# Performance work log

Hardware: AMD Instinct MI355X
Metric: run time of the kernel (lower is better)

Reference implementation:

```python
import jax, jax.numpy as jnp
import numpy as np

LN_EPS = 1e-5

def _layernorm(x, g, b):
    mu = jnp.mean(x, axis=-1, keepdims=True)
    var = jnp.var(x, axis=-1, keepdims=True)
    return (x - mu) * jax.lax.rsqrt(var + LN_EPS) * g + b

def setup_inputs() -> dict:
    key = jax.random.key(0)
    ks = jax.random.split(key, 12)
    B, E, R = 32, 64, 36
    Dt, Di, D = 768, 2048, 512
    s = 0.02
    return {
        "text_feats": jax.random.normal(ks[0], (B, E, Dt), jnp.float32),
        "image_feats": jax.random.normal(ks[1], (B, R, Di), jnp.float32),
        "W_text": jax.random.normal(ks[2], (Dt, D), jnp.float32) * s,
        "b_text": jnp.zeros((D,), jnp.float32),
        "g_text": jnp.ones((D,), jnp.float32),
        "beta_text": jnp.zeros((D,), jnp.float32),
        "W_img": jax.random.normal(ks[3], (Di, D), jnp.float32) * s,
        "b_img": jnp.zeros((D,), jnp.float32),
        "g_img": jnp.ones((D,), jnp.float32),
        "beta_img": jnp.zeros((D,), jnp.float32),
        "W1": jax.random.normal(ks[4], (2 * D, D), jnp.float32) * s,
        "b1": jnp.zeros((D,), jnp.float32),
        "W2": jax.random.normal(ks[5], (D, 1), jnp.float32) * s,
        "b2": jnp.zeros((1,), jnp.float32),
    }

def reference(text_feats, image_feats, W_text, b_text, g_text, beta_text,
              W_img, b_img, g_img, beta_img, W1, b1, W2, b2):
    B, E, _ = text_feats.shape
    R = image_feats.shape[1]
    D = W_text.shape[1]
    # projections: Linear -> ReLU -> LayerNorm
    text_aligned = _layernorm(jax.nn.relu(text_feats @ W_text + b_text), g_text, beta_text)   # [B,E,D]
    image_aligned = _layernorm(jax.nn.relu(image_feats @ W_img + b_img), g_img, beta_img)     # [B,R,D]
    # pairwise scorer: split W1 to avoid materializing the [B,E,R,2D] concat
    W1_t, W1_i = W1[:D], W1[D:]
    h_t = text_aligned @ W1_t                 # [B,E,D]
    h_i = image_aligned @ W1_i + b1           # [B,R,D]
    h = jax.nn.relu(h_t[:, :, None, :] + h_i[:, None, :, :])  # [B,E,R,D]
    scores_raw = jnp.squeeze(h @ W2, -1) + b2[0]               # [B,E,R]
    alignment_scores = jax.nn.sigmoid(scores_raw)
    # softmax over flattened (E*R) per batch
    w = jax.nn.softmax(alignment_scores.reshape(B, E * R), axis=1).reshape(B, E, R)
    # weighted sum over regions, mean over entities
    aggregated = jnp.einsum('ber,brd->bd', w, image_aligned) / E   # [B,D]
    return alignment_scores, aggregated
```

## Files before the change

### kernel.cpp

```cpp
#include <hip/hip_runtime.h>
#include <math.h>

#define LN_EPS 1e-5f

typedef __attribute__((ext_vector_type(8))) short bf16x8;
typedef __attribute__((ext_vector_type(4))) float f32x4;
typedef unsigned short ushort_t;
typedef unsigned int uint_t;

__device__ __forceinline__ ushort_t f2bf(float f) {
    uint_t u = __float_as_uint(f);
    u += 0x7FFF + ((u >> 16) & 1);
    return (ushort_t)(u >> 16);
}

__global__ __launch_bounds__(256) void prep_kernel(
    const float* __restrict__ text, const float* __restrict__ image,
    ushort_t* __restrict__ text_bf, ushort_t* __restrict__ image_bf,
    const float* __restrict__ W_text, const float* __restrict__ W_img,
    const float* __restrict__ W1,
    ushort_t* __restrict__ Wt_t, ushort_t* __restrict__ Wi_t,
    ushort_t* __restrict__ W1t_t, ushort_t* __restrict__ W1i_t)
{
    __shared__ float t[32][33];
    const int bid = blockIdx.x;
    if (bid < 3840) {
        const int i4 = (bid * 256 + threadIdx.x) * 4;
        const float* src; ushort_t* dst; int off;
        if (i4 < 1572864) { src = text;  dst = text_bf;  off = i4; }
        else              { src = image; dst = image_bf; off = i4 - 1572864; }
        float4 v = *(const float4*)(src + off);
        ushort4 o;
        o.x = f2bf(v.x); o.y = f2bf(v.y); o.z = f2bf(v.z); o.w = f2bf(v.w);
        *(ushort4*)(dst + off) = o;
        return;
    }
    int local = bid - 3840;
    const float* src; ushort_t* dst; int K;
    if      (local < 384)  { src = W_text;         dst = Wt_t;  K = 768;  }
    else if (local < 1408) { src = W_img;          dst = Wi_t;  K = 2048; local -= 384; }
    else if (local < 1664) { src = W1;             dst = W1t_t; K = 512;  local -= 1408; }
    else                   { src = W1 + 512 * 512; dst = W1i_t; K = 512;  local -= 1664; }
    const int ntk = K / 32;
    const int k0 = (local % ntk) * 32;
    const int n0 = (local / ntk) * 32;
    const int x = threadIdx.x % 32, y = threadIdx.x / 32;
    #pragma unroll
    for (int j = 0; j < 4; ++j)
        t[y + 8 * j][x] = src[(size_t)(k0 + y + 8 * j) * 512 + n0 + x];
    __syncthreads();
    #pragma unroll
    for (int j = 0; j < 4; ++j)
        dst[(size_t)(n0 + y + 8 * j) * K + k0 + x] = f2bf(t[x][y + 8 * j]);
}

__global__ __launch_bounds__(256) void gemm_splitk_kernel(
    const ushort_t* __restrict__ A0, const ushort_t* __restrict__ B0,
    const float* __restrict__ bias0, float* __restrict__ C0, int K0,
    const ushort_t* __restrict__ A1, const ushort_t* __restrict__ B1,
    const float* __restrict__ bias1, float* __restrict__ C1, int K1,
    int ysplit, int relu)
{
    __shared__ float red[4][64][64];

    const ushort_t* A; const ushort_t* Bt; const float* bias; float* C; int K;
    int yy = blockIdx.y;
    if (yy < ysplit) { A = A0; Bt = B0; bias = bias0; C = C0; K = K0; }
    else { A = A1; Bt = B1; bias = bias1; C = C1; K = K1; yy -= ysplit; }

    const int tid  = threadIdx.x;
    const int wave = tid >> 6;
    const int lane = tid & 63;
    const int q    = lane >> 4;
    const int mj   = lane & 15;
    const int brow = yy * 64;
    const int bcol = blockIdx.x * 64;

    const ushort_t* Ab = A  + (size_t)(brow + mj) * K + q * 8;
    const ushort_t* Bb = Bt + (size_t)(bcol + mj) * K + q * 8;
    const int kw0    = wave * (K >> 2);
    const int ksteps = K >> 7;

    f32x4 acc[4][4] = {};

    #pragma unroll 2
    for (int s = 0; s < ksteps; ++s) {
        const int k = kw0 + s * 32;
        bf16x8 af[4], bf[4];
        #pragma unroll
        for (int i = 0; i < 4; ++i) {
            af[i] = *(const bf16x8*)(Ab + (size_t)i * 16 * K + k);
            bf[i] = *(const bf16x8*)(Bb + (size_t)i * 16 * K + k);
        }
        #pragma unroll
        for (int mi = 0; mi < 4; ++mi)
            #pragma unroll
            for (int ni = 0; ni < 4; ++ni)
                acc[mi][ni] = __builtin_amdgcn_mfma_f32_16x16x32_bf16(
                    af[mi], bf[ni], acc[mi][ni], 0, 0, 0);
    }

    #pragma unroll
    for (int mi = 0; mi < 4; ++mi)
        #pragma unroll
        for (int ni = 0; ni < 4; ++ni)
            #pragma unroll
            for (int r = 0; r < 4; ++r)
                red[wave][mi * 16 + q * 4 + r][ni * 16 + mj] = acc[mi][ni][r];
    __syncthreads();

    #pragma unroll
    for (int g = 0; g < 4; ++g) {
        const int idx = g * 1024 + tid * 4;
        const int row = idx >> 6, col = idx & 63;
        float4 v0 = *(float4*)&red[0][row][col];
        float4 v1 = *(float4*)&red[1][row][col];
        float4 v2 = *(float4*)&red[2][row][col];
        float4 v3 = *(float4*)&red[3][row][col];
        float4 o;
        o.x = (v0.x + v1.x) + (v2.x + v3.x);
        o.y = (v0.y + v1.y) + (v2.y + v3.y);
        o.z = (v0.z + v1.z) + (v2.z + v3.z);
        o.w = (v0.w + v1.w) + (v2.w + v3.w);
        if (bias) {
            float4 bv = *(const float4*)&bias[bcol + col];
            o.x += bv.x; o.y += bv.y; o.z += bv.z; o.w += bv.w;
        }
        if (relu) {
            o.x = fmaxf(o.x, 0.f); o.y = fmaxf(o.y, 0.f);
            o.z = fmaxf(o.z, 0.f); o.w = fmaxf(o.w, 0.f);
        }
        *(float4*)&C[(size_t)(brow + row) * 512 + bcol + col] = o;
    }
}

__global__ __launch_bounds__(256) void ln_fused_kernel(
    float* __restrict__ ta, const float* __restrict__ g_t,
    const float* __restrict__ be_t, ushort_t* __restrict__ ta_bf,
    float* __restrict__ ia, const float* __restrict__ g_i,
    const float* __restrict__ be_i, ushort_t* __restrict__ ia_bf)
{
    const int tid = threadIdx.x;
    int row = blockIdx.x;
    float* p; const float* g; const float* beta; ushort_t* obf; float* ofp;
    if (row < 2048) {
        p = ta + (size_t)row * 512; g = g_t; beta = be_t;
        obf = ta_bf + (size_t)row * 512; ofp = nullptr;
    } else {
        row -= 2048;
        p = ia + (size_t)row * 512; g = g_i; beta = be_i;
        obf = ia_bf + (size_t)row * 512; ofp = p;
    }

    float2 v = *(const float2*)&p[tid * 2];
    float s  = v.x + v.y;
    float ss = v.x * v.x + v.y * v.y;
    #pragma unroll
    for (int off = 32; off; off >>= 1) {
        s  += __shfl_down(s, off);
        ss += __shfl_down(ss, off);
    }
    __shared__ float red[8];
    if ((tid & 63) == 0) { red[(tid >> 6) * 2] = s; red[(tid >> 6) * 2 + 1] = ss; }
    __syncthreads();
    __shared__ float stats[2];
    if (tid == 0) {
        float S  = red[0] + red[2] + red[4] + red[6];
        float SS = red[1] + red[3] + red[5] + red[7];
        float mu  = S * (1.f / 512.f);
        float var = SS * (1.f / 512.f) - mu * mu;
        stats[0] = mu;
        stats[1] = rsqrtf(var + LN_EPS);
    }
    __syncthreads();
    const float mu = stats[0], rstd = stats[1];
    float2 gv = *(const float2*)&g[tid * 2];
    float2 bv = *(const float2*)&beta[tid * 2];
    float o0 = (v.x - mu) * rstd * gv.x + bv.x;
    float o1 = (v.y - mu) * rstd * gv.y + bv.y;
    ushort2 ob; ob.x = f2bf(o0); ob.y = f2bf(o1);
    *(ushort2*)&obf[tid * 2] = ob;
    if (ofp) {
        float2 of; of.x = o0; of.y = o1;
        *(float2*)&ofp[tid * 2] = of;
    }
}

__global__ __launch_bounds__(256) void scores_kernel(
    const float* __restrict__ ht, const float* __restrict__ hi,
    const float* __restrict__ W2, const float* __restrict__ b2,
    float* __restrict__ scores)
{
    const int be   = blockIdx.x;
    const int b    = be >> 6;
    const int tid  = threadIdx.x;
    const int lane = tid & 63;
    const int wave = tid >> 6;

    float htv[8], w2v[8];
    const float* htp = ht + (size_t)be * 512;
    #pragma unroll
    for (int j = 0; j < 8; ++j) {
        htv[j] = htp[lane + 64 * j];
        w2v[j] = W2[lane + 64 * j];
    }
    const float bb = b2[0];
    const float* hib = hi + (size_t)b * 36 * 512;

    for (int r = wave; r < 36; r += 4) {
        const float* hir = hib + (size_t)r * 512;
        float acc = 0.f;
        #pragma unroll
        for (int j = 0; j < 8; ++j) {
            float h = fmaxf(htv[j] + hir[lane + 64 * j], 0.f);
            acc = fmaf(h, w2v[j], acc);
        }
        #pragma unroll
        for (int off = 32; off; off >>= 1) acc += __shfl_down(acc, off);
        if (lane == 0) {
            float sr = acc + bb;
            scores[(size_t)be * 36 + r] = 1.f / (1.f + expf(-sr));
        }
    }
}

__global__ __launch_bounds__(256) void agg_kernel(
    const float* __restrict__ scores, const float* __restrict__ img,
    float* __restrict__ outAgg)
{
    const int b   = blockIdx.x;
    const int tid = threadIdx.x;
    const float* sc = scores + (size_t)b * 2304;

    __shared__ float part[4][36];
    __shared__ float sexp[36];
    __shared__ float inv_s;

    const int e4 = tid >> 6;
    const int r  = tid & 63;
    if (r < 36) {
        float p = 0.f;
        #pragma unroll
        for (int e = 0; e < 16; ++e) p += expf(sc[(e * 4 + e4) * 36 + r]);
        part[e4][r] = p;
    }
    __syncthreads();
    if (tid < 36) sexp[tid] = part[0][tid] + part[1][tid] + part[2][tid] + part[3][tid];
    __syncthreads();
    if (tid < 64) {
        float v = (tid < 36) ? sexp[tid] : 0.f;
        #pragma unroll
        for (int off = 32; off; off >>= 1) v += __shfl_down(v, off);
        if (tid == 0) inv_s = 1.f / (v * 64.f);
    }
    __syncthreads();
    const float inv = inv_s;

    const float* ib = img + (size_t)b * 36 * 512;
    for (int d = tid; d < 512; d += 256) {
        float acc = 0.f;
        #pragma unroll
        for (int rr = 0; rr < 36; ++rr)
            acc = fmaf(sexp[rr] * inv, ib[rr * 512 + d], acc);
        outAgg[(size_t)b * 512 + d] = acc;
    }
}

extern "C" void kernel_launch(void* const* d_in, const int* in_sizes, int n_in,
                              void* d_out, int out_size, void* d_ws, size_t ws_size,
                              hipStream_t stream)
{
    const float* text      = (const float*)d_in[0];
    const float* image     = (const float*)d_in[1];
    const float* W_text    = (const float*)d_in[2];
    const float* b_text    = (const float*)d_in[3];
    const float* g_text    = (const float*)d_in[4];
    const float* beta_text = (const float*)d_in[5];
    const float* W_img     = (const float*)d_in[6];
    const float* b_img     = (const float*)d_in[7];
    const float* g_img     = (const float*)d_in[8];
    const float* beta_img  = (const float*)d_in[9];
    const float* W1        = (const float*)d_in[10];
    const float* b1        = (const float*)d_in[11];
    const float* W2        = (const float*)d_in[12];
    const float* b2        = (const float*)d_in[13];

    float* out_scores = (float*)d_out;
    float* out_agg    = (float*)d_out + 73728;

    char* ws = (char*)d_ws;
    float*    ta       = (float*)(ws);
    float*    ia       = (float*)(ws + (4u << 20));
    ushort_t* text_bf  = (ushort_t*)(ws + 6402048);
    ushort_t* image_bf = (ushort_t*)(ws + 6402048 + 3145728);
    float*    ht       = (float*)(ws + 6402048);
    float*    hi       = (float*)(ws + 6402048 + 4194304);
    char*     wbase    = ws + 6402048 + 7864320;
    ushort_t* Wt_t     = (ushort_t*)(wbase);
    ushort_t* Wi_t     = (ushort_t*)(wbase + 786432);
    ushort_t* W1t_t    = (ushort_t*)(wbase + 786432 + 2097152);
    ushort_t* W1i_t    = (ushort_t*)(wbase + 786432 + 2097152 + 524288);
    char*     bfbase   = wbase + 786432 + 2097152 + 2 * 524288;
    ushort_t* ta_bf    = (ushort_t*)(bfbase);
    ushort_t* ia_bf    = (ushort_t*)(bfbase + 2097152);

    prep_kernel<<<5760, 256, 0, stream>>>(text, image, text_bf, image_bf,
                                          W_text, W_img, W1,
                                          Wt_t, Wi_t, W1t_t, W1i_t);
    gemm_splitk_kernel<<<dim3(8, 50), 256, 0, stream>>>(
        text_bf, Wt_t, b_text, ta, 768,
        image_bf, Wi_t, b_img, ia, 2048,
        32, 1);
    ln_fused_kernel<<<3200, 256, 0, stream>>>(ta, g_text, beta_text, ta_bf,
                                              ia, g_img, beta_img, ia_bf);
    gemm_splitk_kernel<<<dim3(8, 50), 256, 0, stream>>>(
        ta_bf, W1t_t, nullptr, ht, 512,
        ia_bf, W1i_t, b1, hi, 512,
        32, 0);
    scores_kernel<<<2048, 256, 0, stream>>>(ht, hi, W2, b2, out_scores);
    agg_kernel<<<32, 256, 0, stream>>>(out_scores, ia, out_agg);
}
```

Before: 148.0 us.

## Fuse bf16 casts, LayerNorm stats and normalization into GEMM prologues/epilogues

```diff
diff --git a/kernel.cpp b/kernel.cpp
--- a/kernel.cpp
+++ b/kernel.cpp
@@ -14,28 +14,28 @@
     return (ushort_t)(u >> 16);
 }
 
+__device__ __forceinline__ bf16x8 cvt8(float4 a, float4 b) {
+    bf16x8 r;
+    r[0] = (short)f2bf(a.x); r[1] = (short)f2bf(a.y);
+    r[2] = (short)f2bf(a.z); r[3] = (short)f2bf(a.w);
+    r[4] = (short)f2bf(b.x); r[5] = (short)f2bf(b.y);
+    r[6] = (short)f2bf(b.z); r[7] = (short)f2bf(b.w);
+    return r;
+}
+
 __global__ __launch_bounds__(256) void prep_kernel(
-    const float* __restrict__ text, const float* __restrict__ image,
-    ushort_t* __restrict__ text_bf, ushort_t* __restrict__ image_bf,
     const float* __restrict__ W_text, const float* __restrict__ W_img,
     const float* __restrict__ W1,
     ushort_t* __restrict__ Wt_t, ushort_t* __restrict__ Wi_t,
-    ushort_t* __restrict__ W1t_t, ushort_t* __restrict__ W1i_t)
+    ushort_t* __restrict__ W1t_t, ushort_t* __restrict__ W1i_t,
+    float* __restrict__ stats)
 {
     __shared__ float t[32][33];
-    const int bid = blockIdx.x;
-    if (bid < 3840) {
-        const int i4 = (bid * 256 + threadIdx.x) * 4;
-        const float* src; ushort_t* dst; int off;
-        if (i4 < 1572864) { src = text;  dst = text_bf;  off = i4; }
-        else              { src = image; dst = image_bf; off = i4 - 1572864; }
-        float4 v = *(const float4*)(src + off);
-        ushort4 o;
-        o.x = f2bf(v.x); o.y = f2bf(v.y); o.z = f2bf(v.z); o.w = f2bf(v.w);
-        *(ushort4*)(dst + off) = o;
+    int local = blockIdx.x;
+    if (local >= 1920) {
+        for (int i = threadIdx.x; i < 6400; i += 256) stats[i] = 0.f;
         return;
     }
-    int local = bid - 3840;
     const float* src; ushort_t* dst; int K;
     if      (local < 384)  { src = W_text;         dst = Wt_t;  K = 768;  }
     else if (local < 1408) { src = W_img;          dst = Wi_t;  K = 2048; local -= 384; }
@@ -54,19 +54,19 @@
         dst[(size_t)(n0 + y + 8 * j) * K + k0 + x] = f2bf(t[x][y + 8 * j]);
 }
 
-__global__ __launch_bounds__(256) void gemm_splitk_kernel(
-    const ushort_t* __restrict__ A0, const ushort_t* __restrict__ B0,
+__global__ __launch_bounds__(256) void proj_kernel(
+    const float* __restrict__ A0, const ushort_t* __restrict__ B0,
     const float* __restrict__ bias0, float* __restrict__ C0, int K0,
-    const ushort_t* __restrict__ A1, const ushort_t* __restrict__ B1,
+    const float* __restrict__ A1, const ushort_t* __restrict__ B1,
     const float* __restrict__ bias1, float* __restrict__ C1, int K1,
-    int ysplit, int relu)
+    float* __restrict__ stats, int ysplit)
 {
     __shared__ float red[4][64][64];
 
-    const ushort_t* A; const ushort_t* Bt; const float* bias; float* C; int K;
+    const float* A; const ushort_t* Bt; const float* bias; float* C; int K, srow;
     int yy = blockIdx.y;
-    if (yy < ysplit) { A = A0; Bt = B0; bias = bias0; C = C0; K = K0; }
-    else { A = A1; Bt = B1; bias = bias1; C = C1; K = K1; yy -= ysplit; }
+    if (yy < ysplit) { A = A0; Bt = B0; bias = bias0; C = C0; K = K0; srow = yy * 64; }
+    else { A = A1; Bt = B1; bias = bias1; C = C1; K = K1; yy -= ysplit; srow = 2048 + yy * 64; }
 
     const int tid  = threadIdx.x;
     const int wave = tid >> 6;
@@ -76,7 +76,7 @@
     const int brow = yy * 64;
     const int bcol = blockIdx.x * 64;
 
-    const ushort_t* Ab = A  + (size_t)(brow + mj) * K + q * 8;
+    const float*    Ab = A  + (size_t)(brow + mj) * K + q * 8;
     const ushort_t* Bb = Bt + (size_t)(bcol + mj) * K + q * 8;
     const int kw0    = wave * (K >> 2);
     const int ksteps = K >> 7;
@@ -89,7 +89,10 @@
         bf16x8 af[4], bf[4];
         #pragma unroll
         for (int i = 0; i < 4; ++i) {
-            af[i] = *(const bf16x8*)(Ab + (size_t)i * 16 * K + k);
+            const float* pA = Ab + (size_t)i * 16 * K + k;
+            float4 x0 = *(const float4*)pA;
+            float4 x1 = *(const float4*)(pA + 4);
+            af[i] = cvt8(x0, x1);
             bf[i] = *(const bf16x8*)(Bb + (size_t)i * 16 * K + k);
         }
         #pragma unroll
@@ -112,6 +115,118 @@
     #pragma unroll
     for (int g = 0; g < 4; ++g) {
         const int idx = g * 1024 + tid * 4;
+        const int row = idx >> 6, col = idx & 63;
+        float4 v0 = *(float4*)&red[0][row][col];
+        float4 v1 = *(float4*)&red[1][row][col];
+        float4 v2 = *(float4*)&red[2][row][col];
+        float4 v3 = *(float4*)&red[3][row][col];
+        float4 bv = *(const float4*)&bias[bcol + col];
+        float4 o;
+        o.x = fmaxf((v0.x + v1.x) + (v2.x + v3.x) + bv.x, 0.f);
+        o.y = fmaxf((v0.y + v1.y) + (v2.y + v3.y) + bv.y, 0.f);
+        o.z = fmaxf((v0.z + v1.z) + (v2.z + v3.z) + bv.z, 0.f);
+        o.w = fmaxf((v0.w + v1.w) + (v2.w + v3.w) + bv.w, 0.f);
+        *(float4*)&C[(size_t)(brow + row) * 512 + bcol + col] = o;
+        float s  = (o.x + o.y) + (o.z + o.w);
+        float ss = (o.x * o.x + o.y * o.y) + (o.z * o.z + o.w * o.w);
+        #pragma unroll
+        for (int m = 1; m < 16; m <<= 1) {
+            s  += __shfl_xor(s, m);
+            ss += __shfl_xor(ss, m);
+        }
+        if ((tid & 15) == 0) {
+            atomicAdd(&stats[(size_t)(srow + row) * 2], s);
+            atomicAdd(&stats[(size_t)(srow + row) * 2 + 1], ss);
+        }
+    }
+}
+
+__global__ __launch_bounds__(256) void h_kernel(
+    const float* __restrict__ A0, const ushort_t* __restrict__ B0,
+    const float* __restrict__ bias0, float* __restrict__ C0,
+    const float* __restrict__ g0, const float* __restrict__ be0, int soff0,
+    const float* __restrict__ A1, const ushort_t* __restrict__ B1,
+    const float* __restrict__ bias1, float* __restrict__ C1,
+    const float* __restrict__ g1, const float* __restrict__ be1, int soff1,
+    const float* __restrict__ stats, int ysplit)
+{
+    __shared__ float red[4][64][64];
+
+    const float* A; const ushort_t* Bt; const float* bias; float* C;
+    const float* g; const float* be; int soff;
+    int yy = blockIdx.y;
+    if (yy < ysplit) { A = A0; Bt = B0; bias = bias0; C = C0; g = g0; be = be0; soff = soff0; }
+    else { A = A1; Bt = B1; bias = bias1; C = C1; g = g1; be = be1; soff = soff1; yy -= ysplit; }
+
+    const int tid  = threadIdx.x;
+    const int wave = tid >> 6;
+    const int lane = tid & 63;
+    const int q    = lane >> 4;
+    const int mj   = lane & 15;
+    const int brow = yy * 64;
+    const int bcol = blockIdx.x * 64;
+
+    float mu[4], rstd[4];
+    #pragma unroll
+    for (int i = 0; i < 4; ++i) {
+        const int row = soff + brow + i * 16 + mj;
+        float2 st = *(const float2*)&stats[(size_t)row * 2];
+        float m   = st.x * (1.f / 512.f);
+        float var = st.y * (1.f / 512.f) - m * m;
+        mu[i] = m; rstd[i] = rsqrtf(var + LN_EPS);
+    }
+
+    const float*    Ab = A  + (size_t)(brow + mj) * 512 + q * 8;
+    const ushort_t* Bb = Bt + (size_t)(bcol + mj) * 512 + q * 8;
+    const int kw0 = wave * 128;
+
+    f32x4 acc[4][4] = {};
+
+    #pragma unroll 2
+    for (int s = 0; s < 4; ++s) {
+        const int k = kw0 + s * 32;
+        float4 gv0 = *(const float4*)&g[k + q * 8];
+        float4 gv1 = *(const float4*)&g[k + q * 8 + 4];
+        float4 bv0 = *(const float4*)&be[k + q * 8];
+        float4 bv1 = *(const float4*)&be[k + q * 8 + 4];
+        bf16x8 af[4], bf[4];
+        #pragma unroll
+        for (int i = 0; i < 4; ++i) {
+            const float* pA = Ab + (size_t)i * 16 * 512 + k;
+            float4 x0 = *(const float4*)pA;
+            float4 x1 = *(const float4*)(pA + 4);
+            float4 t0, t1;
+            t0.x = fmaf((x0.x - mu[i]) * rstd[i], gv0.x, bv0.x);
+            t0.y = fmaf((x0.y - mu[i]) * rstd[i], gv0.y, bv0.y);
+            t0.z = fmaf((x0.z - mu[i]) * rstd[i], gv0.z, bv0.z);
+            t0.w = fmaf((x0.w - mu[i]) * rstd[i], gv0.w, bv0.w);
+            t1.x = fmaf((x1.x - mu[i]) * rstd[i], gv1.x, bv1.x);
+            t1.y = fmaf((x1.y - mu[i]) * rstd[i], gv1.y, bv1.y);
+            t1.z = fmaf((x1.z - mu[i]) * rstd[i], gv1.z, bv1.z);
+            t1.w = fmaf((x1.w - mu[i]) * rstd[i], gv1.w, bv1.w);
+            af[i] = cvt8(t0, t1);
+            bf[i] = *(const bf16x8*)(Bb + (size_t)i * 16 * 512 + k);
+        }
+        #pragma unroll
+        for (int mi = 0; mi < 4; ++mi)
+            #pragma unroll
+            for (int ni = 0; ni < 4; ++ni)
+                acc[mi][ni] = __builtin_amdgcn_mfma_f32_16x16x32_bf16(
+                    af[mi], bf[ni], acc[mi][ni], 0, 0, 0);
+    }
+
+    #pragma unroll
+    for (int mi = 0; mi < 4; ++mi)
+        #pragma unroll
+        for (int ni = 0; ni < 4; ++ni)
+            #pragma unroll
+            for (int r = 0; r < 4; ++r)
+                red[wave][mi * 16 + q * 4 + r][ni * 16 + mj] = acc[mi][ni][r];
+    __syncthreads();
+
+    #pragma unroll
+    for (int gq = 0; gq < 4; ++gq) {
+        const int idx = gq * 1024 + tid * 4;
         const int row = idx >> 6, col = idx & 63;
         float4 v0 = *(float4*)&red[0][row][col];
         float4 v1 = *(float4*)&red[1][row][col];
@@ -126,63 +241,7 @@
             float4 bv = *(const float4*)&bias[bcol + col];
             o.x += bv.x; o.y += bv.y; o.z += bv.z; o.w += bv.w;
         }
-        if (relu) {
-            o.x = fmaxf(o.x, 0.f); o.y = fmaxf(o.y, 0.f);
-            o.z = fmaxf(o.z, 0.f); o.w = fmaxf(o.w, 0.f);
-        }
         *(float4*)&C[(size_t)(brow + row) * 512 + bcol + col] = o;
-    }
-}
-
-__global__ __launch_bounds__(256) void ln_fused_kernel(
-    float* __restrict__ ta, const float* __restrict__ g_t,
-    const float* __restrict__ be_t, ushort_t* __restrict__ ta_bf,
-    float* __restrict__ ia, const float* __restrict__ g_i,
-    const float* __restrict__ be_i, ushort_t* __restrict__ ia_bf)
-{
-    const int tid = threadIdx.x;
-    int row = blockIdx.x;
-    float* p; const float* g; const float* beta; ushort_t* obf; float* ofp;
-    if (row < 2048) {
-        p = ta + (size_t)row * 512; g = g_t; beta = be_t;
-        obf = ta_bf + (size_t)row * 512; ofp = nullptr;
-    } else {
-        row -= 2048;
-        p = ia + (size_t)row * 512; g = g_i; beta = be_i;
-        obf = ia_bf + (size_t)row * 512; ofp = p;
-    }
-
-    float2 v = *(const float2*)&p[tid * 2];
-    float s  = v.x + v.y;
-    float ss = v.x * v.x + v.y * v.y;
-    #pragma unroll
-    for (int off = 32; off; off >>= 1) {
-        s  += __shfl_down(s, off);
-        ss += __shfl_down(ss, off);
-    }
-    __shared__ float red[8];
-    if ((tid & 63) == 0) { red[(tid >> 6) * 2] = s; red[(tid >> 6) * 2 + 1] = ss; }
-    __syncthreads();
-    __shared__ float stats[2];
-    if (tid == 0) {
-        float S  = red[0] + red[2] + red[4] + red[6];
-        float SS = red[1] + red[3] + red[5] + red[7];
-        float mu  = S * (1.f / 512.f);
-        float var = SS * (1.f / 512.f) - mu * mu;
-        stats[0] = mu;
-        stats[1] = rsqrtf(var + LN_EPS);
-    }
-    __syncthreads();
-    const float mu = stats[0], rstd = stats[1];
-    float2 gv = *(const float2*)&g[tid * 2];
-    float2 bv = *(const float2*)&beta[tid * 2];
-    float o0 = (v.x - mu) * rstd * gv.x + bv.x;
-    float o1 = (v.y - mu) * rstd * gv.y + bv.y;
-    ushort2 ob; ob.x = f2bf(o0); ob.y = f2bf(o1);
-    *(ushort2*)&obf[tid * 2] = ob;
-    if (ofp) {
-        float2 of; of.x = o0; of.y = o1;
-        *(float2*)&ofp[tid * 2] = of;
     }
 }
 
@@ -191,41 +250,59 @@
     const float* __restrict__ W2, const float* __restrict__ b2,
     float* __restrict__ scores)
 {
-    const int be   = blockIdx.x;
-    const int b    = be >> 6;
+    const int blk  = blockIdx.x;
+    const int b    = blk >> 4;
+    const int e0   = (blk & 15) * 4;
     const int tid  = threadIdx.x;
     const int lane = tid & 63;
     const int wave = tid >> 6;
 
-    float htv[8], w2v[8];
-    const float* htp = ht + (size_t)be * 512;
-    #pragma unroll
-    for (int j = 0; j < 8; ++j) {
-        htv[j] = htp[lane + 64 * j];
-        w2v[j] = W2[lane + 64 * j];
-    }
+    float htv[4][8], w2v[8];
+    #pragma unroll
+    for (int e = 0; e < 4; ++e) {
+        const float* htp = ht + (size_t)(b * 64 + e0 + e) * 512;
+        #pragma unroll
+        for (int j = 0; j < 8; ++j) htv[e][j] = htp[lane + 64 * j];
+    }
+    #pragma unroll
+    for (int j = 0; j < 8; ++j) w2v[j] = W2[lane + 64 * j];
     const float bb = b2[0];
     const float* hib = hi + (size_t)b * 36 * 512;
 
     for (int r = wave; r < 36; r += 4) {
         const float* hir = hib + (size_t)r * 512;
-        float acc = 0.f;
+        float hv[8];
+        #pragma unroll
+        for (int j = 0; j < 8; ++j) hv[j] = hir[lane + 64 * j];
+        float a0 = 0.f, a1 = 0.f, a2 = 0.f, a3 = 0.f;
         #pragma unroll
         for (int j = 0; j < 8; ++j) {
-            float h = fmaxf(htv[j] + hir[lane + 64 * j], 0.f);
-            acc = fmaf(h, w2v[j], acc);
-        }
-        #pragma unroll
-        for (int off = 32; off; off >>= 1) acc += __shfl_down(acc, off);
+            a0 = fmaf(fmaxf(htv[0][j] + hv[j], 0.f), w2v[j], a0);
+            a1 = fmaf(fmaxf(htv[1][j] + hv[j], 0.f), w2v[j], a1);
+            a2 = fmaf(fmaxf(htv[2][j] + hv[j], 0.f), w2v[j], a2);
+            a3 = fmaf(fmaxf(htv[3][j] + hv[j], 0.f), w2v[j], a3);
+        }
+        #pragma unroll
+        for (int off = 32; off; off >>= 1) {
+            a0 += __shfl_down(a0, off);
+            a1 += __shfl_down(a1, off);
+            a2 += __shfl_down(a2, off);
+            a3 += __shfl_down(a3, off);
+        }
         if (lane == 0) {
-            float sr = acc + bb;
-            scores[(size_t)be * 36 + r] = 1.f / (1.f + expf(-sr));
+            float* sp = scores + (size_t)(b * 64 + e0) * 36 + r;
+            sp[0]      = 1.f / (1.f + expf(-(a0 + bb)));
+            sp[36]     = 1.f / (1.f + expf(-(a1 + bb)));
+            sp[72]     = 1.f / (1.f + expf(-(a2 + bb)));
+            sp[108]    = 1.f / (1.f + expf(-(a3 + bb)));
         }
     }
 }
 
 __global__ __launch_bounds__(256) void agg_kernel(
-    const float* __restrict__ scores, const float* __restrict__ img,
+    const float* __restrict__ scores, const float* __restrict__ ia_raw,
+    const float* __restrict__ stats2,
+    const float* __restrict__ g, const float* __restrict__ beta,
     float* __restrict__ outAgg)
 {
     const int b   = blockIdx.x;
@@ -233,8 +310,9 @@
     const float* sc = scores + (size_t)b * 2304;
 
     __shared__ float part[4][36];
-    __shared__ float sexp[36];
-    __shared__ float inv_s;
+    __shared__ float wsr[36];
+    __shared__ float tmp[36];
+    __shared__ float inv_s, c1_s;
 
     const int e4 = tid >> 6;
     const int r  = tid & 63;
@@ -245,24 +323,42 @@
         part[e4][r] = p;
     }
     __syncthreads();
-    if (tid < 36) sexp[tid] = part[0][tid] + part[1][tid] + part[2][tid] + part[3][tid];
+    if (tid < 36) wsr[tid] = part[0][tid] + part[1][tid] + part[2][tid] + part[3][tid];
     __syncthreads();
     if (tid < 64) {
-        float v = (tid < 36) ? sexp[tid] : 0.f;
+        float v = (tid < 36) ? wsr[tid] : 0.f;
         #pragma unroll
         for (int off = 32; off; off >>= 1) v += __shfl_down(v, off);
         if (tid == 0) inv_s = 1.f / (v * 64.f);
     }
     __syncthreads();
-    const float inv = inv_s;
-
-    const float* ib = img + (size_t)b * 36 * 512;
+    if (tid < 36) {
+        const int row = b * 36 + tid;
+        float2 st = *(const float2*)&stats2[(size_t)row * 2];
+        float m   = st.x * (1.f / 512.f);
+        float var = st.y * (1.f / 512.f) - m * m;
+        float rs  = rsqrtf(var + LN_EPS);
+        float W   = wsr[tid] * inv_s;
+        wsr[tid]  = W * rs;
+        tmp[tid]  = W * rs * m;
+    }
+    __syncthreads();
+    if (tid < 64) {
+        float v = (tid < 36) ? tmp[tid] : 0.f;
+        #pragma unroll
+        for (int off = 32; off; off >>= 1) v += __shfl_down(v, off);
+        if (tid == 0) c1_s = v;
+    }
+    __syncthreads();
+    const float c1 = c1_s;
+
+    const float* ib = ia_raw + (size_t)b * 36 * 512;
     for (int d = tid; d < 512; d += 256) {
         float acc = 0.f;
         #pragma unroll
         for (int rr = 0; rr < 36; ++rr)
-            acc = fmaf(sexp[rr] * inv, ib[rr * 512 + d], acc);
-        outAgg[(size_t)b * 512 + d] = acc;
+            acc = fmaf(wsr[rr], ib[rr * 512 + d], acc);
+        outAgg[(size_t)b * 512 + d] = g[d] * (acc - c1) + beta[d] * (1.f / 64.f);
     }
 }
 
@@ -289,34 +385,27 @@
     float* out_agg    = (float*)d_out + 73728;
 
     char* ws = (char*)d_ws;
-    float*    ta       = (float*)(ws);
-    float*    ia       = (float*)(ws + (4u << 20));
-    ushort_t* text_bf  = (ushort_t*)(ws + 6402048);
-    ushort_t* image_bf = (ushort_t*)(ws + 6402048 + 3145728);
-    float*    ht       = (float*)(ws + 6402048);
-    float*    hi       = (float*)(ws + 6402048 + 4194304);
-    char*     wbase    = ws + 6402048 + 7864320;
-    ushort_t* Wt_t     = (ushort_t*)(wbase);
-    ushort_t* Wi_t     = (ushort_t*)(wbase + 786432);
-    ushort_t* W1t_t    = (ushort_t*)(wbase + 786432 + 2097152);
-    ushort_t* W1i_t    = (ushort_t*)(wbase + 786432 + 2097152 + 524288);
-    char*     bfbase   = wbase + 786432 + 2097152 + 2 * 524288;
-    ushort_t* ta_bf    = (ushort_t*)(bfbase);
-    ushort_t* ia_bf    = (ushort_t*)(bfbase + 2097152);
-
-    prep_kernel<<<5760, 256, 0, stream>>>(text, image, text_bf, image_bf,
-                                          W_text, W_img, W1,
-                                          Wt_t, Wi_t, W1t_t, W1i_t);
-    gemm_splitk_kernel<<<dim3(8, 50), 256, 0, stream>>>(
-        text_bf, Wt_t, b_text, ta, 768,
-        image_bf, Wi_t, b_img, ia, 2048,
-        32, 1);
-    ln_fused_kernel<<<3200, 256, 0, stream>>>(ta, g_text, beta_text, ta_bf,
-                                              ia, g_img, beta_img, ia_bf);
-    gemm_splitk_kernel<<<dim3(8, 50), 256, 0, stream>>>(
-        ta_bf, W1t_t, nullptr, ht, 512,
-        ia_bf, W1i_t, b1, hi, 512,
-        32, 0);
-    scores_kernel<<<2048, 256, 0, stream>>>(ht, hi, W2, b2, out_scores);
-    agg_kernel<<<32, 256, 0, stream>>>(out_scores, ia, out_agg);
-}
+    float*    ta    = (float*)(ws);
+    float*    ia    = (float*)(ws + 4194304);
+    float*    ht    = (float*)(ws + 6553600);
+    float*    hi    = (float*)(ws + 10747904);
+    ushort_t* Wt_t  = (ushort_t*)(ws + 13107200);
+    ushort_t* Wi_t  = (ushort_t*)(ws + 13893632);
+    ushort_t* W1t_t = (ushort_t*)(ws + 15990784);
+    ushort_t* W1i_t = (ushort_t*)(ws + 16515072);
+    float*    stats = (float*)(ws + 17039360);
+
+    prep_kernel<<<1921, 256, 0, stream>>>(W_text, W_img, W1,
+                                          Wt_t, Wi_t, W1t_t, W1i_t, stats);
+    proj_kernel<<<dim3(8, 50), 256, 0, stream>>>(
+        text, Wt_t, b_text, ta, 768,
+        image, Wi_t, b_img, ia, 2048,
+        stats, 32);
+    h_kernel<<<dim3(8, 50), 256, 0, stream>>>(
+        ta, W1t_t, nullptr, ht, g_text, beta_text, 0,
+        ia, W1i_t, b1, hi, g_img, beta_img, 2048,
+        stats, 32);
+    scores_kernel<<<512, 256, 0, stream>>>(ht, hi, W2, b2, out_scores);
+    agg_kernel<<<32, 256, 0, stream>>>(out_scores, ia, stats + 4096,
+                                       g_img, beta_img, out_agg);
+}
```

Result: slower. 154.3 us (+4.2%).
